# Kernel tuning notes

Hardware: AMD Instinct MI355X
Metric: run time of the kernel (lower is better)

Reference implementation:

```python
import jax, jax.numpy as jnp
import numpy as np

N = 50000       # num nodes
E = 800000      # num edges (avg degree 16)
R = 50          # num relations
F_IN = 768
HID = 256
C = 9
P_DROP = 0.4


def setup_inputs() -> dict:
    key = jax.random.key(0)
    ks = jax.random.split(key, 12)
    x = jax.random.normal(ks[0], (N, F_IN), jnp.float32)
    edge_index = jax.random.randint(ks[1], (2, E), 0, N)
    edge_type = jax.random.randint(ks[2], (E,), 0, R)
    edge_distance = jax.random.uniform(ks[3], (E,), jnp.float32)
    s1 = 1.0 / np.sqrt(F_IN)
    s2 = 1.0 / np.sqrt(HID)
    # RGCNConv params (num_bases=1): basis [B, in, out], comp [R, B], root [in, out], bias [out]
    basis1 = jax.random.normal(ks[4], (1, F_IN, HID), jnp.float32) * s1
    comp1 = jax.random.normal(ks[5], (R, 1), jnp.float32)
    root1 = jax.random.normal(ks[6], (F_IN, HID), jnp.float32) * s1
    bias1 = jnp.zeros((HID,), jnp.float32)
    basis2 = jax.random.normal(ks[7], (1, HID, C), jnp.float32) * s2
    comp2 = jax.random.normal(ks[8], (R, 1), jnp.float32)
    root2 = jax.random.normal(ks[9], (HID, C), jnp.float32) * s2
    bias2 = jnp.zeros((C,), jnp.float32)
    return dict(x=x, edge_index=edge_index, edge_type=edge_type,
                edge_distance=edge_distance,
                basis1=basis1, comp1=comp1, root1=root1, bias1=bias1,
                basis2=basis2, comp2=comp2, root2=root2, bias2=bias2)


def _rgcn_conv(x, edge_index, edge_type, basis, comp, root, bias):
    # PyG RGCNConv with basis decomposition and per-relation mean aggregation.
    src, dst = edge_index[0], edge_index[1]
    n = x.shape[0]
    # project once through bases: [N, B, O]
    hx = jnp.einsum('nf,bfo->nbo', x, basis)
    # per-edge message m_e = sum_b comp[type_e, b] * hx[src_e, b]: [E, O]
    m = jnp.einsum('eb,ebo->eo', comp[edge_type], hx[src])
    # mean aggregation per (dst, relation) pair
    seg = dst * R + edge_type
    cnt = jax.ops.segment_sum(jnp.ones_like(m[:, 0]), seg, num_segments=n * R)
    norm = 1.0 / jnp.maximum(cnt[seg], 1.0)
    out = jax.ops.segment_sum(m * norm[:, None], dst, num_segments=n)
    return out + x @ root + bias


def _dropout(x, key):
    # F.dropout defaults to training=True in the source, so dropout is applied.
    keep = jax.random.bernoulli(key, 1.0 - P_DROP, x.shape)
    return jnp.where(keep, x / (1.0 - P_DROP), 0.0).astype(x.dtype)


def reference(x, edge_index, edge_type, edge_distance,
              basis1, comp1, root1, bias1,
              basis2, comp2, root2, bias2):
    edge_type = edge_type.reshape(-1)
    k1, k2 = jax.random.split(jax.random.key(42))
    h = _rgcn_conv(x, edge_index, edge_type, basis1, comp1, root1, bias1)
    h = jax.nn.relu(_dropout(h, k1))
    h = _rgcn_conv(h, edge_index, edge_type, basis2, comp2, root2, bias2)
    h = jax.nn.relu(_dropout(h, k2))
    return h
```

## Files before the change

kernel.cpp:

```cpp
#include <hip/hip_runtime.h>
#include <stdint.h>
#include <stddef.h>

#define NN 50000
#define NE 800000
#define NR 50
#define FIN 768
#define HD 256
#define NC 9
#define CAP 64

typedef __bf16 bf16x8 __attribute__((ext_vector_type(8)));
typedef float f32x4 __attribute__((ext_vector_type(4)));
typedef unsigned short ushort_t;

__host__ __device__ static inline void tf2x32(uint32_t k0, uint32_t k1,
                                              uint32_t x0, uint32_t x1,
                                              uint32_t& o0, uint32_t& o1) {
  uint32_t ks2 = k0 ^ k1 ^ 0x1BD11BDAu;
  x0 += k0; x1 += k1;
#define TF_R(r) { x0 += x1; x1 = (x1 << r) | (x1 >> (32 - r)); x1 ^= x0; }
  TF_R(13) TF_R(15) TF_R(26) TF_R(6)
  x0 += k1;  x1 += ks2 + 1u;
  TF_R(17) TF_R(29) TF_R(16) TF_R(24)
  x0 += ks2; x1 += k0 + 2u;
  TF_R(13) TF_R(15) TF_R(26) TF_R(6)
  x0 += k0;  x1 += k1 + 3u;
  TF_R(17) TF_R(29) TF_R(16) TF_R(24)
  x0 += k1;  x1 += ks2 + 4u;
  TF_R(13) TF_R(15) TF_R(26) TF_R(6)
  x0 += ks2; x1 += k0 + 5u;
#undef TF_R
  o0 = x0; o1 = x1;
}

__device__ static inline float jax_unif(uint32_t ka, uint32_t kb, uint32_t i) {
  uint32_t o0, o1;
  tf2x32(ka, kb, 0u, i, o0, o1);
  uint32_t bits = o0 ^ o1;
  return __uint_as_float((bits >> 9) | 0x3f800000u) - 1.0f;
}

__device__ static inline float drelu(float v, uint32_t ka, uint32_t kb, uint32_t i) {
  float r = (jax_unif(ka, kb, i) < 0.6f) ? (v * (1.0f / 0.6f)) : 0.0f;
  return fmaxf(r, 0.0f);
}

__device__ static inline uint32_t pk2(float lo, float hi) {
  uint32_t a = (__float_as_uint(lo) + 0x8000u) >> 16;
  uint32_t b = (__float_as_uint(hi) + 0x8000u) & 0xFFFF0000u;
  return a | b;
}
__device__ static inline ushort_t bf1(float v) {
  return (ushort_t)((__float_as_uint(v) + 0x8000u) >> 16);
}
__device__ static inline float ulo(uint32_t u) { return __uint_as_float(u << 16); }
__device__ static inline float uhi(uint32_t u) { return __uint_as_float(u & 0xFFFF0000u); }

__device__ static inline int swz(int r, int s) {
  return r * 64 + ((s ^ ((r >> 1) & 3)) << 4);
}

#define GLDS16(gp, lp) __builtin_amdgcn_global_load_lds(                        \
    (const __attribute__((address_space(1))) void*)(gp),                        \
    (__attribute__((address_space(3))) void*)(lp), 16, 0, 0)


__global__ __launch_bounds__(256) void fillb_k(const int* __restrict__ ei,
                                               const int* __restrict__ et,
                                               const float* __restrict__ basis1,
                                               const float* __restrict__ root1,
                                               unsigned* __restrict__ cursor,
                                               uint2* __restrict__ epw,
                                               ushort_t* __restrict__ Bcat) {
  int gid = blockIdx.x * 256 + threadIdx.x;
  if (gid < NE) {
    int src = ei[gid];
    int dst = ei[NE + gid];
    int t = et[gid];
    unsigned pos = atomicAdd(&cursor[dst], 1u);
    if (pos < CAP)
      epw[(size_t)dst * CAP + pos] =
          make_uint2((uint32_t)src | ((uint32_t)t << 16), 0x3f800000u);
  }
  if (gid < 512 * FIN) {
    int n = gid / FIN, k = gid - n * FIN;
    float v = (n < HD) ? basis1[k * HD + n] : root1[k * HD + (n - HD)];
    Bcat[gid] = bf1(v);
  }
}

__global__ __launch_bounds__(256) void norm_k(const unsigned* __restrict__ cursor,
                                              uint2* __restrict__ epw) {
  int node = blockIdx.x * 4 + (threadIdx.x >> 6);
  int lane = threadIdx.x & 63;
  if (node >= NN) return;
  int d = (int)cursor[node];
  uint2* ep = epw + (size_t)node * CAP;
  uint32_t my = (lane < d) ? ep[lane].x : 0u;
  uint32_t mt = my >> 16;
  int c = 0;
  for (int i = 0; i < d; ++i) {
    uint32_t ti = ep[i].x >> 16;
    c += (ti == mt) ? 1 : 0;
  }
  if (lane < d) ep[lane].y = __float_as_uint(1.0f / (float)c);
}

__global__ __launch_bounds__(256) void mfma_gemm_k(const float* __restrict__ A,
                                                   const ushort_t* __restrict__ Bc,
                                                   ushort_t* __restrict__ C, int M) {
  __shared__ alignas(16) unsigned char ldsA[3][16384];
  __shared__ alignas(16) unsigned char ldsB[3][8192];
  const int K = FIN;
  const int NT = K / 32;

  int id = blockIdx.x;
  int xcd = id & 7, sq = id >> 3;
  int bm128 = xcd + 8 * (sq >> 2);
  if (bm128 >= (M + 127) / 128) return;
  int bm = bm128 * 128;
  int bn = (sq & 3) * 128;

  int t = threadIdx.x;
  int lane = t & 63, w = t >> 6;
  int wm = w >> 1, wn = w & 1;
  int fr = lane & 15, fs = lane >> 4;

  f32x4 acc[4][4];
#pragma unroll
  for (int m = 0; m < 4; ++m)
#pragma unroll
    for (int n = 0; n < 4; ++n) acc[m][n] = (f32x4){0.f, 0.f, 0.f, 0.f};

  int aofE[4], aofO[4], boff[4];
#pragma unroll
  for (int m = 0; m < 4; ++m) {
    int r = wm * 64 + m * 16 + fr;
    aofE[m] = swz(r, fs);
    aofO[m] = 8192 + swz(r, fs);
  }
#pragma unroll
  for (int n = 0; n < 4; ++n) boff[n] = swz(wn * 64 + n * 16 + fr, fs);

  int r0 = t >> 2;
  int l0 = (t & 3) ^ ((r0 >> 1) & 3);
  const float* srcA0 = A + (size_t)min(bm + r0, M - 1) * K + 8 * l0;
  const float* srcA1 = A + (size_t)min(bm + 64 + r0, M - 1) * K + 8 * l0;
  const ushort_t* srcB0 = Bc + (size_t)(bn + r0) * K + l0 * 8;
  const ushort_t* srcB1 = Bc + (size_t)(bn + 64 + r0) * K + l0 * 8;

#define STAGE(bi, k0) {                                                        \
    GLDS16(srcA0 + (k0),     ldsA[bi] + w * 1024);            \
    GLDS16(srcA1 + (k0),     ldsA[bi] + 4096 + w * 1024);     \
    GLDS16(srcA0 + (k0) + 4, ldsA[bi] + 8192 + w * 1024);     \
    GLDS16(srcA1 + (k0) + 4, ldsA[bi] + 12288 + w * 1024);    \
    GLDS16(srcB0 + (k0),     ldsB[bi] + w * 1024);                             \
    GLDS16(srcB1 + (k0),     ldsB[bi] + 4096 + w * 1024); }

  STAGE(0, 0);
  STAGE(1, 32);

  int cur = 0;
  for (int s = 0; s < NT; ++s) {
    if (s < NT - 1) {
      asm volatile("s_waitcnt vmcnt(6)" ::: "memory");
    } else {
      asm volatile("s_waitcnt vmcnt(0)" ::: "memory");
    }
    __builtin_amdgcn_sched_barrier(0);
    __builtin_amdgcn_s_barrier();
    bf16x8 af[4], bfr[4];
#pragma unroll
    for (int m = 0; m < 4; ++m) {
      f32x4 e4 = *(const f32x4*)(ldsA[cur] + aofE[m]);
      f32x4 o4 = *(const f32x4*)(ldsA[cur] + aofO[m]);
      uint4 au;
      au.x = pk2(e4[0], e4[1]); au.y = pk2(e4[2], e4[3]);
      au.z = pk2(o4[0], o4[1]); au.w = pk2(o4[2], o4[3]);
      af[m] = *(bf16x8*)&au;
    }
#pragma unroll
    for (int n = 0; n < 4; ++n) bfr[n] = *(const bf16x8*)(ldsB[cur] + boff[n]);
#pragma unroll
    for (int m = 0; m < 4; ++m)
#pragma unroll
      for (int n = 0; n < 4; ++n)
        acc[m][n] = __builtin_amdgcn_mfma_f32_16x16x32_bf16(af[m], bfr[n],
                                                            acc[m][n], 0, 0, 0);
    if (s + 2 < NT) {
      int nb = cur + 2; if (nb >= 3) nb -= 3;
      STAGE(nb, (s + 2) * 32);
    }
    ++cur; if (cur == 3) cur = 0;
  }
#undef STAGE

#pragma unroll
  for (int m = 0; m < 4; ++m) {
    int rbase = bm + wm * 64 + m * 16 + fs * 4;
#pragma unroll
    for (int r4 = 0; r4 < 4; ++r4) {
      int row = rbase + r4;
      if (row < M) {
        ushort_t* crow = C + (size_t)row * 512 + bn + wn * 64 + fr;
#pragma unroll
        for (int n = 0; n < 4; ++n) crow[n * 16] = bf1(acc[m][n][r4]);
      }
    }
  }
}


__global__ __launch_bounds__(256) void gather1_k(const unsigned* __restrict__ cursor,
                                                 const uint2* __restrict__ epw,
                                                 const float* __restrict__ comp1,
                                                 ushort_t* __restrict__ hxb,
                                                 const float* __restrict__ bias1,
                                                 uint32_t ka, uint32_t kb) {
  __shared__ float cs[NR];
  if (threadIdx.x < NR) cs[threadIdx.x] = comp1[threadIdx.x];
  __syncthreads();
  int node = blockIdx.x * 4 + (threadIdx.x >> 6);
  int lane = threadIdx.x & 63;
  if (node >= NN) return;
  int d = (int)cursor[node];
  const uint2* ep = epw + (size_t)node * CAP;
  float aA0 = 0.f, aA1 = 0.f, aA2 = 0.f, aA3 = 0.f;
  float aB0 = 0.f, aB1 = 0.f, aB2 = 0.f, aB3 = 0.f;
  int j = 0;
  for (; j + 8 <= d; j += 8) {
    uint2 e[8], u[8];
#pragma unroll
    for (int q = 0; q < 8; ++q) e[q] = ep[j + q];
#pragma unroll
    for (int q = 0; q < 8; ++q)
      u[q] = *(const uint2*)(hxb + (size_t)(e[q].x & 0xFFFFu) * 512 + lane * 4);
#pragma unroll
    for (int q = 0; q < 8; ++q) {
      float w_ = cs[e[q].x >> 16] * __uint_as_float(e[q].y);
      if (q & 1) {
        aB0 += w_ * ulo(u[q].x); aB1 += w_ * uhi(u[q].x);
        aB2 += w_ * ulo(u[q].y); aB3 += w_ * uhi(u[q].y);
      } else {
        aA0 += w_ * ulo(u[q].x); aA1 += w_ * uhi(u[q].x);
        aA2 += w_ * ulo(u[q].y); aA3 += w_ * uhi(u[q].y);
      }
    }
  }
  for (; j < d; ++j) {
    uint2 e0 = ep[j];
    uint2 u0 = *(const uint2*)(hxb + (size_t)(e0.x & 0xFFFFu) * 512 + lane * 4);
    float w0 = cs[e0.x >> 16] * __uint_as_float(e0.y);
    aA0 += w0 * ulo(u0.x); aA1 += w0 * uhi(u0.x);
    aA2 += w0 * ulo(u0.y); aA3 += w0 * uhi(u0.y);
  }
  float s0 = aA0 + aB0, s1 = aA1 + aB1, s2 = aA2 + aB2, s3 = aA3 + aB3;
  ushort_t* xrow = hxb + (size_t)node * 512 + 256 + lane * 4;
  uint2 xu = *(const uint2*)xrow;
  float4 b = *(const float4*)(bias1 + lane * 4);
  uint32_t base = (uint32_t)(node * HD + lane * 4);
  float ox = drelu(s0 + ulo(xu.x) + b.x, ka, kb, base + 0);
  float oy = drelu(s1 + uhi(xu.x) + b.y, ka, kb, base + 1);
  float oz = drelu(s2 + ulo(xu.y) + b.z, ka, kb, base + 2);
  float ow = drelu(s3 + uhi(xu.y) + b.w, ka, kb, base + 3);
  *(uint2*)xrow = make_uint2(pk2(ox, oy), pk2(oz, ow));
}

__global__ __launch_bounds__(256) void gemm2_k(const ushort_t* __restrict__ hxb,
                                               const float* __restrict__ basis2,
                                               const float* __restrict__ root2,
                                               float* __restrict__ hxr2) {
  __shared__ float W[256][20];
  int tid = threadIdx.x;
  for (int p = tid; p < 256 * 18; p += 256) {
    int k = p / 18, c = p % 18;
    W[k][c] = (c < 9) ? basis2[k * 9 + c] : root2[k * 9 + (c - 9)];
  }
  __syncthreads();
  int n = blockIdx.x * 256 + tid;
  if (n >= NN) return;
  const ushort_t* hp = hxb + (size_t)n * 512 + 256;
  float acc[18];
#pragma unroll
  for (int c = 0; c < 18; ++c) acc[c] = 0.f;
  for (int k0 = 0; k0 < 256; k0 += 8) {
    uint4 u = *(const uint4*)(hp + k0);
    float f[8];
    f[0] = ulo(u.x); f[1] = uhi(u.x); f[2] = ulo(u.y); f[3] = uhi(u.y);
    f[4] = ulo(u.z); f[5] = uhi(u.z); f[6] = ulo(u.w); f[7] = uhi(u.w);
#pragma unroll
    for (int q = 0; q < 8; ++q)
#pragma unroll
      for (int c = 0; c < 18; ++c) acc[c] += f[q] * W[k0 + q][c];
  }
  float* op = hxr2 + (size_t)n * 20;
#pragma unroll
  for (int c = 0; c < 9; ++c) op[c] = acc[c];
#pragma unroll
  for (int c = 0; c < 9; ++c) op[10 + c] = acc[9 + c];
}

__global__ __launch_bounds__(256) void gather2_k(const unsigned* __restrict__ cursor,
                                                 const uint2* __restrict__ epw,
                                                 const float* __restrict__ comp2,
                                                 const float* __restrict__ hxr2,
                                                 const float* __restrict__ bias2,
                                                 float* __restrict__ out,
                                                 uint32_t ka, uint32_t kb) {
  __shared__ float cs[NR];
  if (threadIdx.x < NR) cs[threadIdx.x] = comp2[threadIdx.x];
  __syncthreads();
  int n = blockIdx.x * 256 + threadIdx.x;
  if (n >= NN) return;
  int d = (int)cursor[n];
  const uint2* ep = epw + (size_t)n * CAP;
  float a[9];
#pragma unroll
  for (int c = 0; c < 9; ++c) a[c] = 0.f;
  int j = 0;
  for (; j + 4 <= d; j += 4) {
    uint2 e[4];
    float4 pa[4], pb[4];
    float pe[4];
#pragma unroll
    for (int q = 0; q < 4; ++q) e[q] = ep[j + q];
#pragma unroll
    for (int q = 0; q < 4; ++q) {
      const float* hp = hxr2 + (size_t)(e[q].x & 0xFFFFu) * 20;
      pa[q] = *(const float4*)hp;
      pb[q] = *(const float4*)(hp + 4);
      pe[q] = hp[8];
    }
#pragma unroll
    for (int q = 0; q < 4; ++q) {
      float w_ = cs[e[q].x >> 16] * __uint_as_float(e[q].y);
      a[0] += w_ * pa[q].x; a[1] += w_ * pa[q].y;
      a[2] += w_ * pa[q].z; a[3] += w_ * pa[q].w;
      a[4] += w_ * pb[q].x; a[5] += w_ * pb[q].y;
      a[6] += w_ * pb[q].z; a[7] += w_ * pb[q].w;
      a[8] += w_ * pe[q];
    }
  }
  for (; j < d; ++j) {
    uint2 e0 = ep[j];
    const float* hp = hxr2 + (size_t)(e0.x & 0xFFFFu) * 20;
    float4 p0a = *(const float4*)hp, p0b = *(const float4*)(hp + 4);
    float p0e = hp[8];
    float w0 = cs[e0.x >> 16] * __uint_as_float(e0.y);
    a[0] += w0 * p0a.x; a[1] += w0 * p0a.y; a[2] += w0 * p0a.z; a[3] += w0 * p0a.w;
    a[4] += w0 * p0b.x; a[5] += w0 * p0b.y; a[6] += w0 * p0b.z; a[7] += w0 * p0b.w;
    a[8] += w0 * p0e;
  }
  const float* xp = hxr2 + (size_t)n * 20 + 10;
#pragma unroll
  for (int c = 0; c < 9; ++c) {
    float v = a[c] + xp[c] + bias2[c];
    out[n * 9 + c] = drelu(v, ka, kb, (uint32_t)(n * 9 + c));
  }
}

extern "C" void kernel_launch(void* const* d_in, const int* in_sizes, int n_in,
                              void* d_out, int out_size, void* d_ws, size_t ws_size,
                              hipStream_t stream) {
  (void)in_sizes; (void)n_in; (void)out_size; (void)ws_size;
  const float* x      = (const float*)d_in[0];
  const int*   ei     = (const int*)d_in[1];
  const int*   et     = (const int*)d_in[2];
  const float* basis1 = (const float*)d_in[4];
  const float* comp1  = (const float*)d_in[5];
  const float* root1  = (const float*)d_in[6];
  const float* bias1  = (const float*)d_in[7];
  const float* basis2 = (const float*)d_in[8];
  const float* comp2  = (const float*)d_in[9];
  const float* root2  = (const float*)d_in[10];
  const float* bias2  = (const float*)d_in[11];
  float* out = (float*)d_out;

  char* ws = (char*)d_ws;
  ushort_t* Bcat   = (ushort_t*)(ws);
  uint2* epw       = (uint2*)(ws + 786432);
  unsigned* cursor = (unsigned*)(ws + 26386432);
  ushort_t* hxb    = (ushort_t*)(ws + 26586560);
  float* hxr2      = (float*)(ws + 77786560);

  uint32_t k1a, k1b, k2a, k2b;
  tf2x32(0u, 42u, 0u, 0u, k1a, k1b);
  tf2x32(0u, 42u, 0u, 1u, k2a, k2b);

  hipMemsetAsync(cursor, 0, 200128, stream);

  fillb_k<<<(NE + 255) / 256, 256, 0, stream>>>(ei, et, basis1, root1, cursor,
                                                epw, Bcat);
  norm_k<<<(NN + 3) / 4, 256, 0, stream>>>(cursor, epw);

  mfma_gemm_k<<<1568, 256, 0, stream>>>(x, Bcat, hxb, NN);

  gather1_k<<<(NN + 3) / 4, 256, 0, stream>>>(cursor, epw, comp1, hxb, bias1,
                                              k1a, k1b);

  gemm2_k<<<(NN + 255) / 256, 256, 0, stream>>>(hxb, basis2, root2, hxr2);

  gather2_k<<<(NN + 255) / 256, 256, 0, stream>>>(cursor, epw, comp2, hxr2,
                                                  bias2, out, k2a, k2b);
}
```

Before: 272.8 us.

## Fuse edge bucketing into GEMM prologue and per-relation counting into gather1

Edge bucketing (the atomic cursor increments and epw writes) moves out of its own kernel and into the start of every block of the MFMA GEMM. The separate norm kernel is removed: gather1 now counts per-relation degrees itself and shares the inverse counts across lanes with shuffles. This drops two kernel launches and one full pass over epw, and lets the scattered atomic traffic overlap with GEMM blocks. In exchange, every GEMM block waits on its atomics before it starts its pipelined loads, and d is now clamped to CAP.

```diff
diff --git a/kernel.cpp b/kernel.cpp
--- a/kernel.cpp
+++ b/kernel.cpp
@@ -66,23 +66,10 @@
     (__attribute__((address_space(3))) void*)(lp), 16, 0, 0)
 
 
-__global__ __launch_bounds__(256) void fillb_k(const int* __restrict__ ei,
-                                               const int* __restrict__ et,
-                                               const float* __restrict__ basis1,
-                                               const float* __restrict__ root1,
-                                               unsigned* __restrict__ cursor,
-                                               uint2* __restrict__ epw,
-                                               ushort_t* __restrict__ Bcat) {
+__global__ __launch_bounds__(256) void bcat_k(const float* __restrict__ basis1,
+                                              const float* __restrict__ root1,
+                                              ushort_t* __restrict__ Bcat) {
   int gid = blockIdx.x * 256 + threadIdx.x;
-  if (gid < NE) {
-    int src = ei[gid];
-    int dst = ei[NE + gid];
-    int t = et[gid];
-    unsigned pos = atomicAdd(&cursor[dst], 1u);
-    if (pos < CAP)
-      epw[(size_t)dst * CAP + pos] =
-          make_uint2((uint32_t)src | ((uint32_t)t << 16), 0x3f800000u);
-  }
   if (gid < 512 * FIN) {
     int n = gid / FIN, k = gid - n * FIN;
     float v = (n < HD) ? basis1[k * HD + n] : root1[k * HD + (n - HD)];
@@ -90,30 +77,34 @@
   }
 }
 
-__global__ __launch_bounds__(256) void norm_k(const unsigned* __restrict__ cursor,
-                                              uint2* __restrict__ epw) {
-  int node = blockIdx.x * 4 + (threadIdx.x >> 6);
-  int lane = threadIdx.x & 63;
-  if (node >= NN) return;
-  int d = (int)cursor[node];
-  uint2* ep = epw + (size_t)node * CAP;
-  uint32_t my = (lane < d) ? ep[lane].x : 0u;
-  uint32_t mt = my >> 16;
-  int c = 0;
-  for (int i = 0; i < d; ++i) {
-    uint32_t ti = ep[i].x >> 16;
-    c += (ti == mt) ? 1 : 0;
-  }
-  if (lane < d) ep[lane].y = __float_as_uint(1.0f / (float)c);
-}
-
 __global__ __launch_bounds__(256) void mfma_gemm_k(const float* __restrict__ A,
                                                    const ushort_t* __restrict__ Bc,
-                                                   ushort_t* __restrict__ C, int M) {
+                                                   ushort_t* __restrict__ C, int M,
+                                                   const int* __restrict__ ei,
+                                                   const int* __restrict__ et,
+                                                   unsigned* __restrict__ cursor,
+                                                   uint2* __restrict__ epw) {
   __shared__ alignas(16) unsigned char ldsA[3][16384];
   __shared__ alignas(16) unsigned char ldsB[3][8192];
   const int K = FIN;
   const int NT = K / 32;
+
+  int t = threadIdx.x;
+
+  {
+    const int EPB = (NE + 1567) / 1568;
+    int e0 = blockIdx.x * EPB;
+    int e1 = min(e0 + EPB, NE);
+    for (int e = e0 + t; e < e1; e += 256) {
+      int src = ei[e];
+      int dst = ei[NE + e];
+      int ty = et[e];
+      unsigned pos = atomicAdd(&cursor[dst], 1u);
+      if (pos < CAP)
+        epw[(size_t)dst * CAP + pos] =
+            make_uint2((uint32_t)src | ((uint32_t)ty << 16), 0u);
+    }
+  }
 
   int id = blockIdx.x;
   int xcd = id & 7, sq = id >> 3;
@@ -122,7 +113,6 @@
   int bm = bm128 * 128;
   int bn = (sq & 3) * 128;
 
-  int t = threadIdx.x;
   int lane = t & 63, w = t >> 6;
   int wm = w >> 1, wn = w & 1;
   int fr = lane & 15, fs = lane >> 4;
@@ -158,6 +148,9 @@
     GLDS16(srcB0 + (k0),     ldsB[bi] + w * 1024);                             \
     GLDS16(srcB1 + (k0),     ldsB[bi] + 4096 + w * 1024); }
 
+  asm volatile("s_waitcnt vmcnt(0)" ::: "memory");
+  __builtin_amdgcn_sched_barrier(0);
+
   STAGE(0, 0);
   STAGE(1, 32);
 
@@ -213,7 +206,7 @@
 
 
 __global__ __launch_bounds__(256) void gather1_k(const unsigned* __restrict__ cursor,
-                                                 const uint2* __restrict__ epw,
+                                                 uint2* __restrict__ epw,
                                                  const float* __restrict__ comp1,
                                                  ushort_t* __restrict__ hxb,
                                                  const float* __restrict__ bias1,
@@ -224,21 +217,28 @@
   int node = blockIdx.x * 4 + (threadIdx.x >> 6);
   int lane = threadIdx.x & 63;
   if (node >= NN) return;
-  int d = (int)cursor[node];
-  const uint2* ep = epw + (size_t)node * CAP;
+  int d = min((int)cursor[node], CAP);
+  uint2* ep = epw + (size_t)node * CAP;
+  uint32_t myx = (lane < d) ? ep[lane].x : 0u;
+  uint32_t mt = myx >> 16;
+  int c = 0;
+  for (int i = 0; i < d; ++i) c += ((ep[i].x >> 16) == mt) ? 1 : 0;
+  float ic = 1.0f / (float)c;
+  if (lane < d) ep[lane].y = __float_as_uint(ic);
   float aA0 = 0.f, aA1 = 0.f, aA2 = 0.f, aA3 = 0.f;
   float aB0 = 0.f, aB1 = 0.f, aB2 = 0.f, aB3 = 0.f;
   int j = 0;
   for (; j + 8 <= d; j += 8) {
-    uint2 e[8], u[8];
-#pragma unroll
-    for (int q = 0; q < 8; ++q) e[q] = ep[j + q];
+    uint32_t ex[8];
+    uint2 u[8];
+#pragma unroll
+    for (int q = 0; q < 8; ++q) ex[q] = ep[j + q].x;
 #pragma unroll
     for (int q = 0; q < 8; ++q)
-      u[q] = *(const uint2*)(hxb + (size_t)(e[q].x & 0xFFFFu) * 512 + lane * 4);
+      u[q] = *(const uint2*)(hxb + (size_t)(ex[q] & 0xFFFFu) * 512 + lane * 4);
 #pragma unroll
     for (int q = 0; q < 8; ++q) {
-      float w_ = cs[e[q].x >> 16] * __uint_as_float(e[q].y);
+      float w_ = cs[ex[q] >> 16] * __shfl(ic, j + q, 64);
       if (q & 1) {
         aB0 += w_ * ulo(u[q].x); aB1 += w_ * uhi(u[q].x);
         aB2 += w_ * ulo(u[q].y); aB3 += w_ * uhi(u[q].y);
@@ -249,9 +249,9 @@
     }
   }
   for (; j < d; ++j) {
-    uint2 e0 = ep[j];
-    uint2 u0 = *(const uint2*)(hxb + (size_t)(e0.x & 0xFFFFu) * 512 + lane * 4);
-    float w0 = cs[e0.x >> 16] * __uint_as_float(e0.y);
+    uint32_t ex = ep[j].x;
+    uint2 u0 = *(const uint2*)(hxb + (size_t)(ex & 0xFFFFu) * 512 + lane * 4);
+    float w0 = cs[ex >> 16] * __shfl(ic, j, 64);
     aA0 += w0 * ulo(u0.x); aA1 += w0 * uhi(u0.x);
     aA2 += w0 * ulo(u0.y); aA3 += w0 * uhi(u0.y);
   }
@@ -313,7 +313,7 @@
   __syncthreads();
   int n = blockIdx.x * 256 + threadIdx.x;
   if (n >= NN) return;
-  int d = (int)cursor[n];
+  int d = min((int)cursor[n], CAP);
   const uint2* ep = epw + (size_t)n * CAP;
   float a[9];
 #pragma unroll
@@ -390,11 +390,9 @@
 
   hipMemsetAsync(cursor, 0, 200128, stream);
 
-  fillb_k<<<(NE + 255) / 256, 256, 0, stream>>>(ei, et, basis1, root1, cursor,
-                                                epw, Bcat);
-  norm_k<<<(NN + 3) / 4, 256, 0, stream>>>(cursor, epw);
-
-  mfma_gemm_k<<<1568, 256, 0, stream>>>(x, Bcat, hxb, NN);
+  bcat_k<<<(512 * FIN + 255) / 256, 256, 0, stream>>>(basis1, root1, Bcat);
+
+  mfma_gemm_k<<<1568, 256, 0, stream>>>(x, Bcat, hxb, NN, ei, et, cursor, epw);
 
   gather1_k<<<(NN + 3) / 4, 256, 0, stream>>>(cursor, epw, comp1, hxb, bias1,
                                               k1a, k1b);
```

New measurement: 247.2 us. 1.1x faster.
